# Kernel optimization log

Measured on AMD Instinct MI355X. Metric: run time of the kernel, lower is better.

Reference implementation:

```python
import jax, jax.numpy as jnp
import numpy as np

CONF_THRES = 0.4
IOU_THRES = 0.45
MAX_DET = 1000
MAX_WH = 7680.0  # class offset for non-agnostic NMS (yolov5 convention)
K = 2048         # pre-NMS candidate cap (>= MAX_DET)


def setup_inputs() -> dict:
    key = jax.random.key(0)
    k1, k2, k3, k4 = jax.random.split(key, 4)
    # uint8-valued image, stored as int32 (values 0..255)
    img = jax.random.randint(k1, (640, 640, 3), 0, 256, dtype=jnp.int32)
    B, N, NC = 8, 25200, 80
    xy = jax.random.uniform(k2, (B, N, 2)) * 640.0          # box centers in pixels
    wh = jax.random.uniform(k3, (B, N, 2)) * 80.0 + 4.0     # box sizes
    sc = jax.random.uniform(k4, (B, N, 1 + NC))             # objectness + class scores
    pred = jnp.concatenate([xy, wh, sc], axis=-1)           # [B, N, 85]
    return {"img": img, "pred": pred}


def _xywh2xyxy(x):
    xy, wh = x[..., :2], x[..., 2:4]
    return jnp.concatenate([xy - wh * 0.5, xy + wh * 0.5], axis=-1)


def _box_iou(a, b):
    # a: [K,4], b: [K,4] in xyxy
    lt = jnp.maximum(a[:, None, :2], b[None, :, :2])
    rb = jnp.minimum(a[:, None, 2:], b[None, :, 2:])
    wh = jnp.clip(rb - lt, 0.0)
    inter = wh[..., 0] * wh[..., 1]
    area_a = (a[:, 2] - a[:, 0]) * (a[:, 3] - a[:, 1])
    area_b = (b[:, 2] - b[:, 0]) * (b[:, 3] - b[:, 1])
    return inter / (area_a[:, None] + area_b[None, :] - inter + 1e-7)


def _nms_single(p):
    # p: [N, 5+nc]
    boxes = _xywh2xyxy(p[:, :4])                 # [N,4]
    conf_all = p[:, 5:] * p[:, 4:5]              # obj * cls
    conf = jnp.max(conf_all, axis=-1)            # best-class confidence [N]
    cls = jnp.argmax(conf_all, axis=-1).astype(p.dtype)
    scores = jnp.where(conf > CONF_THRES, conf, -1.0)
    # top-K candidates (score-sorted, padding gets score -1)
    top_s, idx = jax.lax.top_k(scores, K)
    b = boxes[idx]                               # [K,4] raw boxes
    c = cls[idx]                                 # [K] class ids (float)
    b_off = b + (c * MAX_WH)[:, None]            # class-offset boxes (agnostic_nms=False)
    iou = _box_iou(b_off, b_off)                 # [K,K]
    keep = top_s > CONF_THRES
    ar = jnp.arange(K)

    def body(i, keep):
        sup = keep[i] & (iou[i] > IOU_THRES) & (ar > i)
        return keep & jnp.logical_not(sup)

    keep = jax.lax.fori_loop(0, K, body, keep)
    fs = jnp.where(keep, top_s, -1.0)
    sel_s, sel = jax.lax.top_k(fs, MAX_DET)
    det = jnp.concatenate([b[sel], sel_s[:, None], c[sel][:, None]], axis=-1)  # [MAX_DET,6]
    return jnp.where((sel_s > CONF_THRES)[:, None], det, 0.0)


def reference(img, pred):
    # process_image: HWC -> CHW, BGR->RGB flip, float, /255, add batch dim
    x = img.astype(jnp.float32).transpose(2, 0, 1)[::-1] / 255.0
    x = x[None]                                  # [1,3,640,640]
    det = jax.vmap(_nms_single)(pred)[0]         # non_max_suppression(pred, ...)[0]
    return det, x
```

## Files before the change

### kernel.cpp

```cpp
#include <hip/hip_runtime.h>
#include <stdint.h>

#define N_ANCH 25200
#define NCLS   80
#define KSEL   2048
#define MAXDET 1000
#define CONF_T 0.4f
#define IOU_T  0.45f
#define MAX_WH 7680.0f
#define HBINS  512
#define HBASE  0xBE00u
#define NCAND_MAX 4096
#define NSB    788
#define NIB    400
#define SUPCAP 224
#define RKB    512

#define WS_SELSCORE  0
#define WS_SELBOX    8192
#define WS_DETCAND   40960
#define WS_CNT       92160
#define WS_KEYS      92480
#define WS_CLS       193280
#define WS_MASK      294912
#define WS_MTT       819200
#define WS_F         1343488
#define WS_CAND      294912

__global__ void __launch_bounds__(256)
prep_kernel(const float* __restrict__ pred0, uint32_t* __restrict__ keys,
            int* __restrict__ cls, uint32_t* __restrict__ cnt,
            uint32_t* __restrict__ fglob) {
    int tid = threadIdx.x;
    if (blockIdx.x == 0) {
        if (tid < 64) fglob[tid] = 0u;
        if (tid == 64) *cnt = 0u;
    }
    int lane = tid & 63, wave = tid >> 6;
    int g = lane >> 3, l = lane & 7;
    int a = blockIdx.x * 32 + wave * 8 + g;
    if (a >= N_ANCH) return;
    const float* p = pred0 + (size_t)a * 85;
    float obj = p[4];
    float v = -1e30f; int ci = 0;
    #pragma unroll
    for (int k = 0; k < 10; ++k) {
        int c = l + 8 * k;
        float x = p[5 + c] * obj;
        if (x > v) { v = x; ci = c; }
    }
    #pragma unroll
    for (int m = 1; m < 8; m <<= 1) {
        float ov = __shfl_xor(v, m, 64);
        int   oc = __shfl_xor(ci, m, 64);
        if (ov > v || (ov == v && oc < ci)) { v = ov; ci = oc; }
    }
    if (l == 0) {
        float score = (v > CONF_T) ? v : -1.0f;
        uint32_t bits = __float_as_uint(score);
        uint32_t key = (bits & 0x80000000u) ? ~bits : (bits | 0x80000000u);
        keys[a] = key; cls[a] = ci;
    }
}

__global__ void __launch_bounds__(256)
compact_kernel(const uint32_t* __restrict__ keys, uint32_t* __restrict__ cnt,
               unsigned long long* __restrict__ cand,
               const int* __restrict__ img, float* __restrict__ xout) {
    __shared__ uint32_t h[HBINS];
    __shared__ uint32_t s_lim;
    __shared__ int wtot[4];
    __shared__ int s_base;
    int tid = threadIdx.x;

    if (blockIdx.x >= 25) {
        int i = (blockIdx.x - 25) * 256 + tid;
        const int4* im4 = (const int4*)(img + (size_t)i * 12);
        int4 va = im4[0], vb4 = im4[1], vc = im4[2];
        int p0 = i * 4;
        float4 o0 = make_float4((float)va.z / 255.0f, (float)vb4.y / 255.0f,
                                (float)vc.x / 255.0f, (float)vc.w / 255.0f);
        float4 o1 = make_float4((float)va.y / 255.0f, (float)vb4.x / 255.0f,
                                (float)vb4.w / 255.0f, (float)vc.z / 255.0f);
        float4 o2 = make_float4((float)va.x / 255.0f, (float)va.w / 255.0f,
                                (float)vb4.z / 255.0f, (float)vc.y / 255.0f);
        *(float4*)(xout + p0)          = o0;
        *(float4*)(xout + 409600 + p0) = o1;
        *(float4*)(xout + 819200 + p0) = o2;
        return;
    }

    int lane = tid & 63, wv = tid >> 6;
    for (int b = tid; b < HBINS; b += 256) h[b] = 0u;
    if (tid == 0) s_lim = (HBASE << 16);
    __syncthreads();
    for (int i = tid; i < N_ANCH / 4; i += 256) {
        uint4 kk = ((const uint4*)keys)[i];
        if (kk.x >= (HBASE << 16)) atomicAdd(&h[(kk.x >> 16) - HBASE], 1u);
        if (kk.y >= (HBASE << 16)) atomicAdd(&h[(kk.y >> 16) - HBASE], 1u);
        if (kk.z >= (HBASE << 16)) atomicAdd(&h[(kk.z >> 16) - HBASE], 1u);
        if (kk.w >= (HBASE << 16)) atomicAdd(&h[(kk.w >> 16) - HBASE], 1u);
    }
    __syncthreads();
    for (int off = 1; off < HBINS; off <<= 1) {
        uint32_t a0 = h[tid] + ((tid + off < HBINS) ? h[tid + off] : 0u);
        uint32_t a1 = h[tid + 256] + ((tid + 256 + off < HBINS) ? h[tid + 256 + off] : 0u);
        __syncthreads();
        h[tid] = a0; h[tid + 256] = a1;
        __syncthreads();
    }
    for (int b = tid; b < HBINS; b += 256) {
        uint32_t sb  = h[b];
        uint32_t sb1 = (b < HBINS - 1) ? h[b + 1] : 0u;
        if (sb >= KSEL && sb1 < KSEL) s_lim = (uint32_t)(HBASE + b) << 16;
    }
    __syncthreads();
    uint32_t lim = s_lim;

    int i = blockIdx.x * 256 + tid;
    bool valid = (i < N_ANCH / 4);
    uint32_t ks[4] = {0, 0, 0, 0};
    int cm = 0;
    if (valid) {
        uint4 kk = ((const uint4*)keys)[i];
        ks[0] = kk.x; ks[1] = kk.y; ks[2] = kk.z; ks[3] = kk.w;
        #pragma unroll
        for (int j = 0; j < 4; ++j) cm += (ks[j] >= lim) ? 1 : 0;
    }
    int pre = cm;
    #pragma unroll
    for (int o = 1; o < 64; o <<= 1) {
        int v = __shfl_up(pre, o, 64);
        if (lane >= o) pre += v;
    }
    if (lane == 63) wtot[wv] = pre;
    __syncthreads();
    if (tid == 0) {
        int t = 0;
        #pragma unroll
        for (int w = 0; w < 4; ++w) { int x = wtot[w]; wtot[w] = t; t += x; }
        s_base = (t > 0) ? (int)atomicAdd(cnt, (uint32_t)t) : 0;
    }
    __syncthreads();
    int pos = s_base + wtot[wv] + (pre - cm);
    if (valid) {
        #pragma unroll
        for (int j = 0; j < 4; ++j) {
            if (ks[j] >= lim) {
                if (pos < NCAND_MAX)
                    cand[pos] = ((unsigned long long)ks[j] << 32)
                              | (uint32_t)(~(uint32_t)(i * 4 + j));
                ++pos;
            }
        }
    }
}

__global__ void __launch_bounds__(256)
rank_kernel(const uint32_t* __restrict__ cnt, const unsigned long long* __restrict__ cand,
            const float* __restrict__ pred0, const int* __restrict__ cls,
            float* __restrict__ sel_score, float4* __restrict__ selbox,
            float* __restrict__ det_cand) {
    __shared__ unsigned long long s_it[NCAND_MAX];
    __shared__ int s_n;
    int tid = threadIdx.x;
    if (tid == 0) s_n = (int)min(*cnt, (uint32_t)NCAND_MAX);
    __syncthreads();
    int n = s_n;
    int base = blockIdx.x * 8;
    if (base >= n) return;
    #pragma unroll 4
    for (int i = tid; i < n; i += 256) s_it[i] = cand[i];
    __syncthreads();
    int grp = tid >> 5, s32 = tid & 31;
    int it = base + grp;
    if (it < n) {
        unsigned long long mine = s_it[it];
        int c = 0;
        #pragma unroll 8
        for (int t = s32; t < n; t += 32)
            c += (s_it[t] > mine) ? 1 : 0;
        #pragma unroll
        for (int m = 1; m < 32; m <<= 1) c += __shfl_xor(c, m, 64);
        if (s32 == 0 && c < KSEL) {
            uint32_t key = (uint32_t)(mine >> 32);
            int ai = (int)(~(uint32_t)mine);
            uint32_t fb = (key & 0x80000000u) ? (key & 0x7FFFFFFFu) : ~key;
            float score = __uint_as_float(fb);
            const float* p = pred0 + (size_t)ai * 85;
            float x = p[0], y = p[1], w = p[2], hh = p[3];
            float x1 = x - w * 0.5f, y1 = y - hh * 0.5f;
            float x2 = x + w * 0.5f, y2 = y + hh * 0.5f;
            float cf = (float)cls[ai];
            float off = cf * MAX_WH;
            selbox[c] = make_float4(x1 + off, y1 + off, x2 + off, y2 + off);
            float* dc = det_cand + (size_t)c * 6;
            dc[0] = x1; dc[1] = y1; dc[2] = x2; dc[3] = y2; dc[4] = score; dc[5] = cf;
            sel_score[c] = score;
        }
    }
}

__global__ void __launch_bounds__(256)
mask_kernel(const float4* __restrict__ selbox, uint32_t* __restrict__ MT,
            uint32_t* __restrict__ MTT, uint32_t* __restrict__ fglob) {
    __shared__ float4 jb[32];
    int tid = threadIdx.x;
    int lane = tid & 63, wv = tid >> 6;
    int wi = blockIdx.x >> 3, rg = blockIdx.x & 7;

    if (tid < 32) jb[tid] = selbox[wi * 32 + tid];
    __syncthreads();
    int row = rg * 256 + tid;
    float4 a = selbox[row];
    float areaA = (a.z - a.x) * (a.w - a.y);
    uint32_t bits = 0;
    #pragma unroll 4
    for (int b = 0; b < 32; ++b) {
        int j = wi * 32 + b;
        if (j > row) {
            float4 q = jb[b];
            float lx = fmaxf(a.x, q.x), ly = fmaxf(a.y, q.y);
            float rx = fminf(a.z, q.z), ry = fminf(a.w, q.w);
            float ww = fmaxf(rx - lx, 0.0f), hh = fmaxf(ry - ly, 0.0f);
            float inter = ww * hh;
            float areaB = (q.z - q.x) * (q.w - q.y);
            float iou = inter / (areaA + areaB - inter + 1e-7f);
            if (iou > IOU_T) bits |= (1u << b);
        }
    }
    MT[(size_t)wi * 2048 + row] = bits;
    MTT[(size_t)row * 64 + wi] = bits;
    unsigned long long bm = __ballot(bits != 0u);
    if (lane == 0) {
        int wbase = rg * 8 + wv * 2;
        uint32_t lo = (uint32_t)bm, hi = (uint32_t)(bm >> 32);
        if (lo) atomicOr(&fglob[wbase], lo);
        if (hi) atomicOr(&fglob[wbase + 1], hi);
    }
}

__global__ void __launch_bounds__(256)
nms_kernel(const uint32_t* __restrict__ MT, const uint32_t* __restrict__ MTT,
           const uint32_t* __restrict__ fglob, const float* __restrict__ sel_score,
           const float* __restrict__ det_cand, float* __restrict__ det) {
    __shared__ __align__(16) uint32_t sup[SUPCAP * 64];
    __shared__ uint32_t f_s[64];
    __shared__ int rowlist[SUPCAP];
    __shared__ int s_R;
    int tid = threadIdx.x;

    if (tid < 64) {
        uint32_t fw = fglob[tid];
        f_s[tid] = fw;
        int cnt1 = __popc(fw);
        int pre = cnt1;
        for (int o = 1; o < 64; o <<= 1) {
            int v = __shfl_up(pre, o, 64);
            if (tid >= o) pre += v;
        }
        int r = pre - cnt1;
        while (fw) {
            int b = __ffs(fw) - 1; fw &= fw - 1;
            if (r < SUPCAP) rowlist[r] = tid * 32 + b;
            ++r;
        }
        if (tid == 63) s_R = pre;
    }
    __syncthreads();
    int R = s_R;
    bool sparse = (R <= SUPCAP);
    if (sparse) {
        int s = tid >> 6, ln = tid & 63;
        while (s + 12 < R) {
            uint32_t a0 = MTT[(size_t)rowlist[s]      * 64 + ln];
            uint32_t a1 = MTT[(size_t)rowlist[s + 4]  * 64 + ln];
            uint32_t a2 = MTT[(size_t)rowlist[s + 8]  * 64 + ln];
            uint32_t a3 = MTT[(size_t)rowlist[s + 12] * 64 + ln];
            sup[s * 64 + ln] = a0;        sup[(s + 4) * 64 + ln] = a1;
            sup[(s + 8) * 64 + ln] = a2;  sup[(s + 12) * 64 + ln] = a3;
            s += 16;
        }
        for (; s < R; s += 4)
            sup[s * 64 + ln] = MTT[(size_t)rowlist[s] * 64 + ln];
    }
    __syncthreads();
    if (tid >= 64) return;

    int lane = tid;
    uint32_t removed = 0;
    #pragma unroll
    for (int b = 0; b < 32; ++b)
        if (!(sel_score[lane * 32 + b] > CONF_T)) removed |= (1u << b);

    if (sparse) {
        int slot = 0;
        for (int w = 0; w < 64; ++w) {
            uint32_t fb = f_s[w];
            while (fb) {
                int b = __ffs(fb) - 1; fb &= fb - 1;
                uint32_t rv = __shfl((int)removed, w, 64);
                if (!((rv >> b) & 1u))
                    removed |= sup[slot * 64 + lane];
                ++slot;
            }
        }
    } else {
        for (int c = 0; c < 64; ++c) {
            uint32_t rw[32];
            #pragma unroll 8
            for (int b = 0; b < 32; ++b)
                rw[b] = MT[(size_t)lane * 2048 + c * 32 + b];
            uint32_t keptmask = 0;
            if (lane == c) {
                uint32_t myrem = removed;
                #pragma unroll
                for (int b = 0; b < 32; ++b)
                    if (!((myrem >> b) & 1u)) { keptmask |= (1u << b); myrem |= rw[b]; }
            }
            keptmask = __shfl(keptmask, c, 64);
            #pragma unroll
            for (int b = 0; b < 32; ++b)
                if ((keptmask >> b) & 1u) removed |= rw[b];
        }
    }

    uint32_t kw = ~removed;
    int cnt2 = __popc(kw);
    int pre = cnt2;
    for (int o = 1; o < 64; o <<= 1) {
        int v = __shfl_up(pre, o, 64);
        if (lane >= o) pre += v;
    }
    int excl = pre - cnt2;
    int total = __shfl(pre, 63, 64);

    int r = excl;
    for (int b = 0; b < 32; ++b) {
        if ((kw >> b) & 1u) {
            if (r < MAXDET) {
                const float* src = det_cand + (size_t)(lane * 32 + b) * 6;
                float* dst = det + (size_t)r * 6;
                for (int j = 0; j < 6; ++j) dst[j] = src[j];
            }
            ++r;
        }
    }
    int start = total < MAXDET ? total : MAXDET;
    for (int z = start + lane; z < MAXDET; z += 64) {
        float* dst = det + (size_t)z * 6;
        for (int j = 0; j < 6; ++j) dst[j] = 0.0f;
    }
}

extern "C" void kernel_launch(void* const* d_in, const int* in_sizes, int n_in,
                              void* d_out, int out_size, void* d_ws, size_t ws_size,
                              hipStream_t stream) {
    const int*   img  = (const int*)d_in[0];
    const float* pred = (const float*)d_in[1];
    float* out = (float*)d_out;
    char* ws = (char*)d_ws;

    float*    sel_score = (float*)(ws + WS_SELSCORE);
    float4*   selbox    = (float4*)(ws + WS_SELBOX);
    float*    det_cand  = (float*)(ws + WS_DETCAND);
    uint32_t* cnt       = (uint32_t*)(ws + WS_CNT);
    uint32_t* keys      = (uint32_t*)(ws + WS_KEYS);
    int*      cls       = (int*)(ws + WS_CLS);
    uint32_t* MT        = (uint32_t*)(ws + WS_MASK);
    uint32_t* MTT       = (uint32_t*)(ws + WS_MTT);
    uint32_t* fglob     = (uint32_t*)(ws + WS_F);
    unsigned long long* cand = (unsigned long long*)(ws + WS_CAND);
    float* xout = out + MAXDET * 6;

    prep_kernel<<<NSB, 256, 0, stream>>>(pred, keys, cls, cnt, fglob);
    compact_kernel<<<25 + NIB, 256, 0, stream>>>(keys, cnt, cand, img, xout);
    rank_kernel<<<RKB, 256, 0, stream>>>(cnt, cand, pred, cls,
                                         sel_score, selbox, det_cand);
    mask_kernel<<<512, 256, 0, stream>>>(selbox, MT, MTT, fglob);
    nms_kernel<<<1, 256, 0, stream>>>(MT, MTT, fglob, sel_score, det_cand, out);
}
```

Baseline: 134.7 us.

## Fuse scoring, compaction, and histogram into one kernel; rank does threshold compaction

The scoring kernel now compacts above-threshold anchors directly into a rough candidate list and builds a global histogram with atomics, and it also does the image conversion. This removes the separate compact kernel and one launch. Each of the 512 rank blocks rebuilds the cutoff from the histogram and re-filters the rough list into shared memory. The class id is packed into the candidate key, and the nms kernel resets the global counters for the next call. The trade-off is that every rank block redundantly scans the rough list, which could hold roughly 15k+ entries for these inputs, and global histogram atomics contend.

```diff
diff --git a/kernel.cpp b/kernel.cpp
--- a/kernel.cpp
+++ b/kernel.cpp
@@ -15,66 +15,29 @@
 #define NIB    400
 #define SUPCAP 224
 #define RKB    512
+#define ROUGH_MAX 25216
 
 #define WS_SELSCORE  0
 #define WS_SELBOX    8192
 #define WS_DETCAND   40960
-#define WS_CNT       92160
-#define WS_KEYS      92480
-#define WS_CLS       193280
-#define WS_MASK      294912
-#define WS_MTT       819200
-#define WS_F         1343488
-#define WS_CAND      294912
+#define WS_ROUGH     98304
+#define WS_MASK      327680
+#define WS_MTT       851968
+#define WS_F         1376256
+
+__device__ uint32_t g_cnt;
+__device__ uint32_t g_hist[HBINS];
 
 __global__ void __launch_bounds__(256)
-prep_kernel(const float* __restrict__ pred0, uint32_t* __restrict__ keys,
-            int* __restrict__ cls, uint32_t* __restrict__ cnt,
-            uint32_t* __restrict__ fglob) {
+prep_img_kernel(const float* __restrict__ pred0, const int* __restrict__ img,
+                float* __restrict__ xout, unsigned long long* __restrict__ rough,
+                uint32_t* __restrict__ fglob) {
     int tid = threadIdx.x;
-    if (blockIdx.x == 0) {
-        if (tid < 64) fglob[tid] = 0u;
-        if (tid == 64) *cnt = 0u;
-    }
-    int lane = tid & 63, wave = tid >> 6;
-    int g = lane >> 3, l = lane & 7;
-    int a = blockIdx.x * 32 + wave * 8 + g;
-    if (a >= N_ANCH) return;
-    const float* p = pred0 + (size_t)a * 85;
-    float obj = p[4];
-    float v = -1e30f; int ci = 0;
-    #pragma unroll
-    for (int k = 0; k < 10; ++k) {
-        int c = l + 8 * k;
-        float x = p[5 + c] * obj;
-        if (x > v) { v = x; ci = c; }
-    }
-    #pragma unroll
-    for (int m = 1; m < 8; m <<= 1) {
-        float ov = __shfl_xor(v, m, 64);
-        int   oc = __shfl_xor(ci, m, 64);
-        if (ov > v || (ov == v && oc < ci)) { v = ov; ci = oc; }
-    }
-    if (l == 0) {
-        float score = (v > CONF_T) ? v : -1.0f;
-        uint32_t bits = __float_as_uint(score);
-        uint32_t key = (bits & 0x80000000u) ? ~bits : (bits | 0x80000000u);
-        keys[a] = key; cls[a] = ci;
-    }
-}
-
-__global__ void __launch_bounds__(256)
-compact_kernel(const uint32_t* __restrict__ keys, uint32_t* __restrict__ cnt,
-               unsigned long long* __restrict__ cand,
-               const int* __restrict__ img, float* __restrict__ xout) {
-    __shared__ uint32_t h[HBINS];
-    __shared__ uint32_t s_lim;
-    __shared__ int wtot[4];
-    __shared__ int s_base;
-    int tid = threadIdx.x;
-
-    if (blockIdx.x >= 25) {
-        int i = (blockIdx.x - 25) * 256 + tid;
+    int bid = blockIdx.x;
+    if (bid == 0 && tid < 64) fglob[tid] = 0u;
+
+    if (bid >= NSB) {
+        int i = (bid - NSB) * 256 + tid;
         const int4* im4 = (const int4*)(img + (size_t)i * 12);
         int4 va = im4[0], vb4 = im4[1], vc = im4[2];
         int p0 = i * 4;
@@ -90,17 +53,64 @@
         return;
     }
 
-    int lane = tid & 63, wv = tid >> 6;
-    for (int b = tid; b < HBINS; b += 256) h[b] = 0u;
+    __shared__ int wtot[4];
+    __shared__ int s_base;
+    int lane = tid & 63, wave = tid >> 6;
+    int g = lane >> 3, l = lane & 7;
+    int a = bid * 32 + wave * 8 + g;
+    bool valid = (a < N_ANCH);
+    float v = -1e30f; int ci = 0;
+    if (valid) {
+        const float* p = pred0 + (size_t)a * 85;
+        float obj = p[4];
+        #pragma unroll
+        for (int k = 0; k < 10; ++k) {
+            int c = l + 8 * k;
+            float x = p[5 + c] * obj;
+            if (x > v) { v = x; ci = c; }
+        }
+        #pragma unroll
+        for (int m = 1; m < 8; m <<= 1) {
+            float ov = __shfl_xor(v, m, 64);
+            int   oc = __shfl_xor(ci, m, 64);
+            if (ov > v || (ov == v && oc < ci)) { v = ov; ci = oc; }
+        }
+    }
+    bool cand = valid && (l == 0) && (v > CONF_T);
+    unsigned long long bm = __ballot(cand);
+    if (lane == 0) wtot[wave] = __popcll(bm);
+    __syncthreads();
+    if (tid == 0) {
+        int t = 0;
+        #pragma unroll
+        for (int w = 0; w < 4; ++w) { int x = wtot[w]; wtot[w] = t; t += x; }
+        s_base = (t > 0) ? (int)atomicAdd(&g_cnt, (uint32_t)t) : 0;
+    }
+    __syncthreads();
+    if (cand) {
+        uint32_t key = __float_as_uint(v) | 0x80000000u;
+        int pos = s_base + wtot[wave]
+                + (int)__popcll(bm & ((1ull << (g * 8)) - 1ull));
+        rough[pos] = ((unsigned long long)key << 32)
+                   | (uint32_t)~(((uint32_t)a << 7) | (uint32_t)ci);
+        atomicAdd(&g_hist[(key >> 16) - HBASE], 1u);
+    }
+}
+
+__global__ void __launch_bounds__(256)
+rank_kernel(const unsigned long long* __restrict__ rough,
+            const float* __restrict__ pred0, float* __restrict__ sel_score,
+            float4* __restrict__ selbox, float* __restrict__ det_cand) {
+    __shared__ uint32_t h[HBINS];
+    __shared__ unsigned long long s_it[NCAND_MAX];
+    __shared__ uint32_t s_lim;
+    __shared__ int wt4[4];
+    __shared__ int s_n;
+    int tid = threadIdx.x, lane = tid & 63, wv = tid >> 6;
+    int cnt = (int)g_cnt;
+
+    h[tid] = g_hist[tid]; h[tid + 256] = g_hist[tid + 256];
     if (tid == 0) s_lim = (HBASE << 16);
-    __syncthreads();
-    for (int i = tid; i < N_ANCH / 4; i += 256) {
-        uint4 kk = ((const uint4*)keys)[i];
-        if (kk.x >= (HBASE << 16)) atomicAdd(&h[(kk.x >> 16) - HBASE], 1u);
-        if (kk.y >= (HBASE << 16)) atomicAdd(&h[(kk.y >> 16) - HBASE], 1u);
-        if (kk.z >= (HBASE << 16)) atomicAdd(&h[(kk.z >> 16) - HBASE], 1u);
-        if (kk.w >= (HBASE << 16)) atomicAdd(&h[(kk.w >> 16) - HBASE], 1u);
-    }
     __syncthreads();
     for (int off = 1; off < HBINS; off <<= 1) {
         uint32_t a0 = h[tid] + ((tid + off < HBINS) ? h[tid + off] : 0u);
@@ -117,65 +127,44 @@
     __syncthreads();
     uint32_t lim = s_lim;
 
-    int i = blockIdx.x * 256 + tid;
-    bool valid = (i < N_ANCH / 4);
-    uint32_t ks[4] = {0, 0, 0, 0};
-    int cm = 0;
-    if (valid) {
-        uint4 kk = ((const uint4*)keys)[i];
-        ks[0] = kk.x; ks[1] = kk.y; ks[2] = kk.z; ks[3] = kk.w;
-        #pragma unroll
-        for (int j = 0; j < 4; ++j) cm += (ks[j] >= lim) ? 1 : 0;
-    }
-    int pre = cm;
+    int my = 0;
+    #pragma unroll 4
+    for (int i = tid; i < cnt; i += 256)
+        my += ((uint32_t)(rough[i] >> 32) >= lim) ? 1 : 0;
+    int pre = my;
     #pragma unroll
     for (int o = 1; o < 64; o <<= 1) {
         int v = __shfl_up(pre, o, 64);
         if (lane >= o) pre += v;
     }
-    if (lane == 63) wtot[wv] = pre;
+    if (lane == 63) wt4[wv] = pre;
     __syncthreads();
     if (tid == 0) {
         int t = 0;
         #pragma unroll
-        for (int w = 0; w < 4; ++w) { int x = wtot[w]; wtot[w] = t; t += x; }
-        s_base = (t > 0) ? (int)atomicAdd(cnt, (uint32_t)t) : 0;
-    }
-    __syncthreads();
-    int pos = s_base + wtot[wv] + (pre - cm);
-    if (valid) {
-        #pragma unroll
-        for (int j = 0; j < 4; ++j) {
-            if (ks[j] >= lim) {
-                if (pos < NCAND_MAX)
-                    cand[pos] = ((unsigned long long)ks[j] << 32)
-                              | (uint32_t)(~(uint32_t)(i * 4 + j));
-                ++pos;
-            }
-        }
-    }
-}
-
-__global__ void __launch_bounds__(256)
-rank_kernel(const uint32_t* __restrict__ cnt, const unsigned long long* __restrict__ cand,
-            const float* __restrict__ pred0, const int* __restrict__ cls,
-            float* __restrict__ sel_score, float4* __restrict__ selbox,
-            float* __restrict__ det_cand) {
-    __shared__ unsigned long long s_it[NCAND_MAX];
-    __shared__ int s_n;
-    int tid = threadIdx.x;
-    if (tid == 0) s_n = (int)min(*cnt, (uint32_t)NCAND_MAX);
-    __syncthreads();
-    int n = s_n;
+        for (int w = 0; w < 4; ++w) { int x = wt4[w]; wt4[w] = t; t += x; }
+        s_n = t;
+    }
+    __syncthreads();
+    int n = min(s_n, NCAND_MAX);
     int base = blockIdx.x * 8;
     if (base >= n) return;
+
+    int pos = wt4[wv] + (pre - my);
     #pragma unroll 4
-    for (int i = tid; i < n; i += 256) s_it[i] = cand[i];
-    __syncthreads();
+    for (int i = tid; i < cnt; i += 256) {
+        unsigned long long it = rough[i];
+        if ((uint32_t)(it >> 32) >= lim) {
+            if (pos < NCAND_MAX) s_it[pos] = it;
+            ++pos;
+        }
+    }
+    __syncthreads();
+
     int grp = tid >> 5, s32 = tid & 31;
-    int it = base + grp;
-    if (it < n) {
-        unsigned long long mine = s_it[it];
+    int it_i = base + grp;
+    if (it_i < n) {
+        unsigned long long mine = s_it[it_i];
         int c = 0;
         #pragma unroll 8
         for (int t = s32; t < n; t += 32)
@@ -184,14 +173,15 @@
         for (int m = 1; m < 32; m <<= 1) c += __shfl_xor(c, m, 64);
         if (s32 == 0 && c < KSEL) {
             uint32_t key = (uint32_t)(mine >> 32);
-            int ai = (int)(~(uint32_t)mine);
-            uint32_t fb = (key & 0x80000000u) ? (key & 0x7FFFFFFFu) : ~key;
-            float score = __uint_as_float(fb);
+            uint32_t u = ~(uint32_t)mine;
+            int ai = (int)(u >> 7);
+            int ci = (int)(u & 127u);
+            float score = __uint_as_float(key & 0x7FFFFFFFu);
             const float* p = pred0 + (size_t)ai * 85;
             float x = p[0], y = p[1], w = p[2], hh = p[3];
             float x1 = x - w * 0.5f, y1 = y - hh * 0.5f;
             float x2 = x + w * 0.5f, y2 = y + hh * 0.5f;
-            float cf = (float)cls[ai];
+            float cf = (float)ci;
             float off = cf * MAX_WH;
             selbox[c] = make_float4(x1 + off, y1 + off, x2 + off, y2 + off);
             float* dc = det_cand + (size_t)c * 6;
@@ -249,6 +239,9 @@
     __shared__ int rowlist[SUPCAP];
     __shared__ int s_R;
     int tid = threadIdx.x;
+
+    g_hist[tid] = 0u; g_hist[tid + 256] = 0u;
+    if (tid == 0) g_cnt = 0u;
 
     if (tid < 64) {
         uint32_t fw = fglob[tid];
@@ -364,19 +357,14 @@
     float*    sel_score = (float*)(ws + WS_SELSCORE);
     float4*   selbox    = (float4*)(ws + WS_SELBOX);
     float*    det_cand  = (float*)(ws + WS_DETCAND);
-    uint32_t* cnt       = (uint32_t*)(ws + WS_CNT);
-    uint32_t* keys      = (uint32_t*)(ws + WS_KEYS);
-    int*      cls       = (int*)(ws + WS_CLS);
+    unsigned long long* rough = (unsigned long long*)(ws + WS_ROUGH);
     uint32_t* MT        = (uint32_t*)(ws + WS_MASK);
     uint32_t* MTT       = (uint32_t*)(ws + WS_MTT);
     uint32_t* fglob     = (uint32_t*)(ws + WS_F);
-    unsigned long long* cand = (unsigned long long*)(ws + WS_CAND);
     float* xout = out + MAXDET * 6;
 
-    prep_kernel<<<NSB, 256, 0, stream>>>(pred, keys, cls, cnt, fglob);
-    compact_kernel<<<25 + NIB, 256, 0, stream>>>(keys, cnt, cand, img, xout);
-    rank_kernel<<<RKB, 256, 0, stream>>>(cnt, cand, pred, cls,
-                                         sel_score, selbox, det_cand);
+    prep_img_kernel<<<NSB + NIB, 256, 0, stream>>>(pred, img, xout, rough, fglob);
+    rank_kernel<<<RKB, 256, 0, stream>>>(rough, pred, sel_score, selbox, det_cand);
     mask_kernel<<<512, 256, 0, stream>>>(selbox, MT, MTT, fglob);
     nms_kernel<<<1, 256, 0, stream>>>(MT, MTT, fglob, sel_score, det_cand, out);
 }
```

After: 161.3 us. +19.7%, slower.
